# Kernel optimization log

Measured on AMD Instinct MI355X. Metric: run time of the kernel, lower is better.

The kernel has to match this reference:

```python
import jax, jax.numpy as jnp
import numpy as np

B, S, HID = 2, 2048, 3072
NH, NKV, HD = 24, 8, 128  # num_heads, kv heads, head_dim
G = NH // NKV             # GQA group size = 3
SCALING = HD ** -0.5
LAYER_SCALING = 1.0       # sqrt(layer_number=1)


def setup_inputs() -> dict:
    key = jax.random.key(0)
    ks = jax.random.split(key, 10)
    std = 0.02
    inp = {
        "hidden_states": jax.random.normal(ks[0], (B, S, HID), jnp.float32),
        # additive causal mask: 0 on/below diag, -1e9 above
        "attention_mask": jnp.where(
            jnp.tril(jnp.ones((S, S), bool)), 0.0, -1e9
        ).astype(jnp.float32)[None, None],
        # torch nn.Linear layout: W is [out, in]
        "Wq": jax.random.normal(ks[1], (HID, HID), jnp.float32) * std,
        "bq": jnp.zeros((HID,), jnp.float32),
        "Wk": jax.random.normal(ks[2], (NKV * HD, HID), jnp.float32) * std,
        "bk": jnp.zeros((NKV * HD,), jnp.float32),
        "Wv": jax.random.normal(ks[3], (NKV * HD, HID), jnp.float32) * std,
        "bv": jnp.zeros((NKV * HD,), jnp.float32),
        "Wd": jax.random.normal(ks[4], (HID, HID), jnp.float32) * std,
        "bd": jnp.zeros((HID,), jnp.float32),
    }
    return inp


def reference(hidden_states, attention_mask, Wq, bq, Wk, bk, Wv, bv, Wd, bd):
    b, s, _ = hidden_states.shape
    q = hidden_states @ Wq.T + bq                     # [B,S,HID]
    k = hidden_states @ Wk.T + bk                     # [B,S,NKV*HD]
    v = hidden_states @ Wv.T + bv
    # grouped layout: q [B,NKV,G,S,D]; repeat_interleave(dim=1) == grouped kv head
    q = q.reshape(b, s, NKV, G, HD).transpose(0, 2, 3, 1, 4)
    k = k.reshape(b, s, NKV, HD).transpose(0, 2, 1, 3)  # [B,NKV,S,D]
    v = v.reshape(b, s, NKV, HD).transpose(0, 2, 1, 3)
    scores = jnp.einsum("bhgqd,bhkd->bhgqk", q, k)
    scores = scores * (SCALING / LAYER_SCALING)
    scores = scores + attention_mask[:, :, None]       # broadcast over kv-head/group
    probs = jax.nn.softmax(scores.astype(jnp.float32), axis=-1).astype(scores.dtype)
    ctx = jnp.einsum("bhgqk,bhkd->bhgqd", probs, v)    # [B,NKV,G,S,D]
    # (kv_head, group) flattened == repeat_interleave head ordering
    ctx = ctx.transpose(0, 3, 1, 2, 4).reshape(b, s, HID)
    return ctx @ Wd.T + bd
```

## Files before the change

### kernel.cpp

```cpp
#include <hip/hip_runtime.h>

typedef unsigned short ushort_t;
typedef unsigned int uint32;
typedef __bf16 bf16x8 __attribute__((ext_vector_type(8)));
typedef float f32x4 __attribute__((ext_vector_type(4)));
typedef float f32x16 __attribute__((ext_vector_type(16)));

#define MFMA16(a, b, c) __builtin_amdgcn_mfma_f32_16x16x32_bf16((a), (b), (c), 0, 0, 0)
#define MFMA32(a, b, c) __builtin_amdgcn_mfma_f32_32x32x16_bf16((a), (b), (c), 0, 0, 0)

__device__ __forceinline__ ushort_t f2bf(float f) {
  union { float f; uint32 u; } c; c.f = f;
  uint32 u = c.u;
  u += 0x7fffu + ((u >> 16) & 1u);
  return (ushort_t)(u >> 16);
}

__device__ __forceinline__ void gload_lds16(const void* g, void* l) {
  __builtin_amdgcn_global_load_lds(
      (const __attribute__((address_space(1))) void*)g,
      (__attribute__((address_space(3))) void*)l, 16, 0, 0);
}

__global__ __launch_bounds__(256)
void cvt5_kernel(const float* __restrict__ p0, const float* __restrict__ p1,
                 const float* __restrict__ p2, const float* __restrict__ p3,
                 const float* __restrict__ p4, ushort_t* __restrict__ out) {
  const size_t B0 = 12582912;
  const size_t B1 = B0 + 9437184;
  const size_t B2 = B1 + 3145728;
  const size_t B3 = B2 + 3145728;
  const size_t B4 = B3 + 9437184;
  const size_t step = (size_t)gridDim.x * 256 * 4;
  for (size_t g = ((size_t)blockIdx.x * 256 + threadIdx.x) * 4; g < B4; g += step) {
    const float* src; size_t off;
    if (g < B0)      { src = p0; off = 0;  }
    else if (g < B1) { src = p1; off = B0; }
    else if (g < B2) { src = p2; off = B1; }
    else if (g < B3) { src = p3; off = B2; }
    else             { src = p4; off = B3; }
    float4 v = *(const float4*)(src + (g - off));
    union { uint2 u; ushort_t s[4]; } p;
    p.s[0] = f2bf(v.x); p.s[1] = f2bf(v.y);
    p.s[2] = f2bf(v.z); p.s[3] = f2bf(v.w);
    *(uint2*)(out + g) = p.u;
  }
}

#define GEMM_BODY32(ABASE, WROWBASE, KD)                                        \
  f32x16 acc[2][2] = {};                                                        \
  const int l31 = lane & 31;                                                    \
  const int khb = (lane >> 5) << 4;            \
  const int nk = (KD) >> 6;                                                     \
  for (int kt = 0; kt < nk; ++kt) {                                             \
    _Pragma("unroll")                                                           \
    for (int i = 0; i < 4; ++i) {                                               \
      int o = (i * 256 + tid) * 16;                                             \
      int row = o >> 7;                                                         \
      int src = (o & 127) ^ ((row & 7) << 4);                                   \
      gload_lds16(ABASE + (rowA0 + row) * (KD) + kt * 64 + (src >> 1),          \
                  (char*)As + o);                                               \
      gload_lds16(WROWBASE + (size_t)row * (KD) + kt * 64 + (src >> 1),         \
                  (char*)Bs + o);                                               \
    }                                                                           \
    __syncthreads();                                                            \
    _Pragma("unroll")                                                           \
    for (int ks = 0; ks < 4; ++ks) {                                            \
      bf16x8 af[2], bfr[2];                                                     \
      _Pragma("unroll")                                                         \
      for (int mi = 0; mi < 2; ++mi) {                                          \
        int ar = wr * 64 + mi * 32 + l31;                                       \
        int off = ar * 128 + ((ks * 32 + khb) ^ ((ar & 7) << 4));               \
        af[mi] = *(const bf16x8*)((const char*)As + off);                       \
      }                                                                         \
      _Pragma("unroll")                                                         \
      for (int nj = 0; nj < 2; ++nj) {                                          \
        int br = wc * 64 + nj * 32 + l31;                                       \
        int off = br * 128 + ((ks * 32 + khb) ^ ((br & 7) << 4));               \
        bfr[nj] = *(const bf16x8*)((const char*)Bs + off);                      \
      }                                                                         \
      _Pragma("unroll")                                                         \
      for (int mi = 0; mi < 2; ++mi)                                            \
        _Pragma("unroll")                                                       \
        for (int nj = 0; nj < 2; ++nj)                                          \
          acc[mi][nj] = MFMA32(af[mi], bfr[nj], acc[mi][nj]);                   \
    }                                                                           \
    __syncthreads();                                                            \
  }

__global__ __launch_bounds__(256)
void qkv_gemm_kernel(const ushort_t* __restrict__ A,
                     const ushort_t* __restrict__ Wq, const ushort_t* __restrict__ Wk,
                     const ushort_t* __restrict__ Wv,
                     const float* __restrict__ bq, const float* __restrict__ bk,
                     const float* __restrict__ bv, ushort_t* __restrict__ C)
{
  __shared__ __attribute__((aligned(16))) ushort_t As[128 * 64];
  __shared__ __attribute__((aligned(16))) ushort_t Bs[128 * 64];
  const int tid = threadIdx.x;
  const int lane = tid & 63;
  const int wv_ = tid >> 6;
  const int wr = wv_ >> 1, wc = wv_ & 1;
  const int x = blockIdx.x & 7;
  const int li = blockIdx.x >> 3;
  const int bm = ((x & 1) << 4) | (li & 15);
  const int bn = (x >> 1) * 10 + (li >> 4);

  const ushort_t* Wsrc; const float* bsrc; int nloc;
  if (bn < 24)      { Wsrc = Wq; bsrc = bq; nloc = bn << 7; }
  else if (bn < 32) { Wsrc = Wk; bsrc = bk; nloc = (bn - 24) << 7; }
  else              { Wsrc = Wv; bsrc = bv; nloc = (bn - 32) << 7; }

  const size_t rowA0 = (size_t)bm * 128;
  const ushort_t* Wrow = Wsrc + (size_t)nloc * 3072;

  GEMM_BODY32(A, Wrow, 3072)

  const int rhi = (lane >> 5) << 2;
#pragma unroll
  for (int nj = 0; nj < 2; ++nj) {
    int cl = wc * 64 + nj * 32 + l31;
    float bvl = bsrc[nloc + cl];
    int col = bn * 128 + cl;
#pragma unroll
    for (int mi = 0; mi < 2; ++mi) {
      int row0 = bm * 128 + wr * 64 + mi * 32 + rhi;
#pragma unroll
      for (int r = 0; r < 16; ++r) {
        int rowl = (r & 3) + 8 * (r >> 2);
        C[(size_t)(row0 + rowl) * 5120 + col] = f2bf(acc[mi][nj][r] + bvl);
      }
    }
  }
}

template <bool OUT_F32>
__global__ __launch_bounds__(256)
void gemm_bt_kernel(const ushort_t* __restrict__ A, const ushort_t* __restrict__ W,
                    const float* __restrict__ bias, void* __restrict__ Cv,
                    int N, int Kd, int cbn)
{
  __shared__ __attribute__((aligned(16))) ushort_t As[128 * 64];
  __shared__ __attribute__((aligned(16))) ushort_t Bs[128 * 64];
  const int tid = threadIdx.x;
  const int lane = tid & 63;
  const int wv_ = tid >> 6;
  const int wr = wv_ >> 1, wc = wv_ & 1;
  const int x = blockIdx.x & 7;
  const int li = blockIdx.x >> 3;
  const int bm = ((x & 1) << 4) | (li & 15);
  const int bn = (x >> 1) * cbn + (li >> 4);

  const size_t rowA0 = (size_t)bm * 128;
  const ushort_t* Wrow = W + (size_t)(bn * 128) * Kd;

  GEMM_BODY32(A, Wrow, Kd)

  const int rhi = (lane >> 5) << 2;
#pragma unroll
  for (int nj = 0; nj < 2; ++nj) {
    int col = bn * 128 + wc * 64 + nj * 32 + l31;
    float bvl = bias[col];
#pragma unroll
    for (int mi = 0; mi < 2; ++mi) {
      int row0 = bm * 128 + wr * 64 + mi * 32 + rhi;
#pragma unroll
      for (int r = 0; r < 16; ++r) {
        int rowl = (r & 3) + 8 * (r >> 2);
        float v = acc[mi][nj][r] + bvl;
        if (OUT_F32) ((float*)Cv)[(size_t)(row0 + rowl) * N + col] = v;
        else         ((ushort_t*)Cv)[(size_t)(row0 + rowl) * N + col] = f2bf(v);
      }
    }
  }
}

#define NHEADS 24
#define GRP 3
#define SEQ 2048
#define QSCL 0.12751745f
#define DTHR 8.0f

__global__ __launch_bounds__(256)
void attn_kernel(const ushort_t* __restrict__ QKV, ushort_t* __restrict__ O)
{
  __shared__ __attribute__((aligned(16))) ushort_t Kl[2][64 * 128];
  __shared__ __attribute__((aligned(16))) ushort_t Vt[128 * 64];

  const int tid = threadIdx.x;
  const int lane = tid & 63;
  const int wv = tid >> 6;
  const int l15 = lane & 15, lg = lane >> 4;
  const int bh = blockIdx.x;
  const int qb = 31 - blockIdx.y;
  const int b = bh / NHEADS, h = bh % NHEADS;
  const int kvh = h / GRP;
  const size_t kbase = (size_t)b * SEQ * 5120 + 3072 + (size_t)kvh * 128;
  const size_t vbase = kbase + 1024;
  const int q0 = qb * 64;

  const int kv4 = (tid & 15) * 4;
  const int d8 = (tid >> 4) * 8;
  const int a_sel = lg >> 1;
  const int s0l = (lane & 15) + 32 * (lg & 1);

#pragma unroll
  for (int i = 0; i < 4; ++i) {
    int o = (i * 256 + tid) * 16;
    int row = o >> 8;
    int src = (o & 255) ^ ((row & 7) << 4);
    gload_lds16(QKV + kbase + (size_t)row * 5120 + (src >> 1), (char*)&Kl[0][0] + o);
  }
  uint4 vr0, vr1, vr2, vr3;
  {
    const ushort_t* vg = QKV + vbase + (size_t)kv4 * 5120 + d8;
    vr0 = *(const uint4*)(vg);
    vr1 = *(const uint4*)(vg + 5120);
    vr2 = *(const uint4*)(vg + 10240);
    vr3 = *(const uint4*)(vg + 15360);
  }

  bf16x8 qf[4];
  {
    const ushort_t* qg = QKV + (size_t)(b * SEQ + q0 + wv * 16 + l15) * 5120 + h * 128 + lg * 8;
#pragma unroll
    for (int c = 0; c < 4; ++c) {
      bf16x8 q = *(const bf16x8*)(qg + c * 32);
#pragma unroll
      for (int e = 0; e < 8; ++e) q[e] = (__bf16)((float)q[e] * QSCL);
      qf[c] = q;
    }
  }

  float m_st = -1e30f, l_st = 0.f;
  f32x4 accO[8] = {};

  for (int t = 0; t <= qb; ++t) {
    const int cur = t & 1;
    {
      union { uint4 u; ushort_t s[8]; } L0, L1, L2, L3;
      L0.u = vr0; L1.u = vr1; L2.u = vr2; L3.u = vr3;
#pragma unroll
      for (int dd = 0; dd < 8; ++dd) {
        int d = d8 + dd;
        uint2 w;
        w.x = (uint32)L0.s[dd] | ((uint32)L1.s[dd] << 16);
        w.y = (uint32)L2.s[dd] | ((uint32)L3.s[dd] << 16);
        int swz = ((d & 7) ^ ((d >> 3) & 3)) << 4;
        int off = (d * 128 + kv4 * 2) ^ swz;
        *(uint2*)((char*)Vt + off) = w;
      }
    }
    asm volatile("s_waitcnt lgkmcnt(0)" ::: "memory");
    __builtin_amdgcn_s_barrier();

    if (t < qb) {
      const int kvn = (t + 1) * 64;
#pragma unroll
      for (int i = 0; i < 4; ++i) {
        int o = (i * 256 + tid) * 16;
        int row = o >> 8;
        int src = (o & 255) ^ ((row & 7) << 4);
        gload_lds16(QKV + kbase + (size_t)(kvn + row) * 5120 + (src >> 1),
                    (char*)&Kl[cur ^ 1][0] + o);
      }
      const ushort_t* vg = QKV + vbase + (size_t)(kvn + kv4) * 5120 + d8;
      vr0 = *(const uint4*)(vg);
      vr1 = *(const uint4*)(vg + 5120);
      vr2 = *(const uint4*)(vg + 10240);
      vr3 = *(const uint4*)(vg + 15360);
    }

    f32x4 s[4];
    __builtin_amdgcn_s_setprio(1);
#pragma unroll
    for (int n = 0; n < 4; ++n) {
      f32x4 z = {0.f, 0.f, 0.f, 0.f};
      s[n] = z;
#pragma unroll
      for (int c = 0; c < 4; ++c) {
        int row = n * 16 + l15;
        int boff = (row * 256 + c * 64 + lg * 16) ^ ((row & 7) << 4);
        bf16x8 kf = *(const bf16x8*)((const char*)Kl[cur] + boff);
        s[n] = MFMA16(kf, qf[c], s[n]);
      }
    }
    __builtin_amdgcn_s_setprio(0);

    if (t == qb) {
      const int qg_ = wv * 16 + l15;
#pragma unroll
      for (int n = 0; n < 4; ++n)
#pragma unroll
        for (int r = 0; r < 4; ++r)
          if (n * 16 + lg * 4 + r > qg_) s[n][r] = -1e9f;
    }

    float mx = fmaxf(fmaxf(fmaxf(s[0][0], s[0][1]), fmaxf(s[0][2], s[0][3])),
                     fmaxf(fmaxf(s[1][0], s[1][1]), fmaxf(s[1][2], s[1][3])));
    mx = fmaxf(mx, fmaxf(fmaxf(fmaxf(s[2][0], s[2][1]), fmaxf(s[2][2], s[2][3])),
                         fmaxf(fmaxf(s[3][0], s[3][1]), fmaxf(s[3][2], s[3][3]))));
    mx = fmaxf(mx, __shfl_xor(mx, 16, 64));
    mx = fmaxf(mx, __shfl_xor(mx, 32, 64));

    if (!__all(mx <= m_st + DTHR)) {
      const float mnew = fmaxf(m_st, mx);
      const float alpha = __builtin_amdgcn_exp2f(m_st - mnew);
      m_st = mnew;
      l_st *= alpha;
#pragma unroll
      for (int j = 0; j < 8; ++j)
#pragma unroll
        for (int r = 0; r < 4; ++r) accO[j][r] *= alpha;
    }

    float rsum = 0.f;
    uint32 dwA[4], dwB[4];
#pragma unroll
    for (int n = 0; n < 4; ++n) {
      float p0 = __builtin_amdgcn_exp2f(s[n][0] - m_st);
      float p1 = __builtin_amdgcn_exp2f(s[n][1] - m_st);
      float p2 = __builtin_amdgcn_exp2f(s[n][2] - m_st);
      float p3 = __builtin_amdgcn_exp2f(s[n][3] - m_st);
      rsum += (p0 + p1) + (p2 + p3);
      dwA[n] = (uint32)f2bf(p0) | ((uint32)f2bf(p1) << 16);
      dwB[n] = (uint32)f2bf(p2) | ((uint32)f2bf(p3) << 16);
    }
    rsum += __shfl_xor(rsum, 16, 64);
    rsum += __shfl_xor(rsum, 32, 64);
    l_st += rsum;

#pragma unroll
    for (int c = 0; c < 2; ++c) {
      uint32 xA0 = __shfl((int)dwA[2 * c],     s0l,      64);
      uint32 xB0 = __shfl((int)dwB[2 * c],     s0l,      64);
      uint32 xA1 = __shfl((int)dwA[2 * c + 1], s0l,      64);
      uint32 xB1 = __shfl((int)dwB[2 * c + 1], s0l,      64);
      uint32 yA0 = __shfl((int)dwA[2 * c],     s0l + 16, 64);
      uint32 yB0 = __shfl((int)dwB[2 * c],     s0l + 16, 64);
      uint32 yA1 = __shfl((int)dwA[2 * c + 1], s0l + 16, 64);
      uint32 yB1 = __shfl((int)dwB[2 * c + 1], s0l + 16, 64);
      union { uint4 u; bf16x8 v; } pb;
      pb.u.x = a_sel ? xA1 : xA0;
      pb.u.y = a_sel ? xB1 : xB0;
      pb.u.z = a_sel ? yA1 : yA0;
      pb.u.w = a_sel ? yB1 : yB0;
      __builtin_amdgcn_s_setprio(1);
#pragma unroll
      for (int j = 0; j < 8; ++j) {
        int d = j * 16 + l15;
        int swz = ((d & 7) ^ ((d >> 3) & 3)) << 4;
        int off = (d * 128 + c * 64 + lg * 16) ^ swz;
        bf16x8 vf = *(const bf16x8*)((const char*)Vt + off);
        accO[j] = MFMA16(vf, pb.v, accO[j]);
      }
      __builtin_amdgcn_s_setprio(0);
    }
    __builtin_amdgcn_s_barrier();
  }

  const float inv = 1.0f / l_st;
  ushort_t* og = O + (size_t)(b * SEQ + q0 + wv * 16 + l15) * 3072 + h * 128 + lg * 4;
#pragma unroll
  for (int j = 0; j < 8; ++j) {
    union { uint2 u; ushort_t s[4]; } w;
    w.s[0] = f2bf(accO[j][0] * inv);
    w.s[1] = f2bf(accO[j][1] * inv);
    w.s[2] = f2bf(accO[j][2] * inv);
    w.s[3] = f2bf(accO[j][3] * inv);
    *(uint2*)(og + j * 16) = w.u;
  }
}

extern "C" void kernel_launch(void* const* d_in, const int* in_sizes, int n_in,
                              void* d_out, int out_size, void* d_ws, size_t ws_size,
                              hipStream_t stream) {
  const float* hs = (const float*)d_in[0];
  const float* Wq = (const float*)d_in[2];
  const float* bq = (const float*)d_in[3];
  const float* Wk = (const float*)d_in[4];
  const float* bk = (const float*)d_in[5];
  const float* Wv = (const float*)d_in[6];
  const float* bv = (const float*)d_in[7];
  const float* Wd = (const float*)d_in[8];
  const float* bd = (const float*)d_in[9];
  float* out = (float*)d_out;

  const size_t N_HS = (size_t)4096 * 3072;
  const size_t N_WQ = (size_t)3072 * 3072;
  const size_t N_WK = (size_t)1024 * 3072;

  ushort_t* hs_bf = (ushort_t*)d_ws;
  ushort_t* Wq_bf = hs_bf + N_HS;
  ushort_t* Wk_bf = Wq_bf + N_WQ;
  ushort_t* Wv_bf = Wk_bf + N_WK;
  ushort_t* Wd_bf = Wv_bf + N_WK;
  ushort_t* QKVw  = Wd_bf + N_WQ;
  ushort_t* Cw    = hs_bf;

  cvt5_kernel<<<dim3(2048), dim3(256), 0, stream>>>(hs, Wq, Wk, Wv, Wd, hs_bf);
  qkv_gemm_kernel<<<dim3(1280), dim3(256), 0, stream>>>(hs_bf, Wq_bf, Wk_bf, Wv_bf,
                                                        bq, bk, bv, QKVw);
  attn_kernel<<<dim3(48, 32), dim3(256), 0, stream>>>(QKVw, Cw);
  gemm_bt_kernel<true><<<dim3(24 * 32), dim3(256), 0, stream>>>(Cw, Wd_bf, bd, out,
                                                                3072, 3072, 6);
}
```

Measured before the change: 395.2 us.

## Permute K rows in LDS so QK^T output feeds PV MFMA without shuffles

Loads K tile rows into LDS in a permuted order (kperm), so each lane's S accumulator elements already sit in the B-operand layout the P·V MFMA expects. This removes the eight cross-lane shuffles and selects per chunk, and the causal mask index is recomputed to match the permuted key order. It also swaps the manual f2bf rounding for native __bf16 conversions in the P packing and the output store. The risk is a wrong permutation or mask mapping, which would silently corrupt the attention result.

```diff
diff --git a/kernel.cpp b/kernel.cpp
--- a/kernel.cpp
+++ b/kernel.cpp
@@ -181,6 +181,10 @@
 #define QSCL 0.12751745f
 #define DTHR 8.0f
 
+__device__ __forceinline__ int kperm(int u) {
+  return 8 * ((u >> 2) & 3) + 4 * ((u >> 4) & 1) + (u & 3) + 32 * (u >> 5);
+}
+
 __global__ __launch_bounds__(256)
 void attn_kernel(const ushort_t* __restrict__ QKV, ushort_t* __restrict__ O)
 {
@@ -201,15 +205,14 @@
 
   const int kv4 = (tid & 15) * 4;
   const int d8 = (tid >> 4) * 8;
-  const int a_sel = lg >> 1;
-  const int s0l = (lane & 15) + 32 * (lg & 1);
 
 #pragma unroll
   for (int i = 0; i < 4; ++i) {
     int o = (i * 256 + tid) * 16;
     int row = o >> 8;
     int src = (o & 255) ^ ((row & 7) << 4);
-    gload_lds16(QKV + kbase + (size_t)row * 5120 + (src >> 1), (char*)&Kl[0][0] + o);
+    gload_lds16(QKV + kbase + (size_t)kperm(row) * 5120 + (src >> 1),
+                (char*)&Kl[0][0] + o);
   }
   uint4 vr0, vr1, vr2, vr3;
   {
@@ -261,7 +264,7 @@
         int o = (i * 256 + tid) * 16;
         int row = o >> 8;
         int src = (o & 255) ^ ((row & 7) << 4);
-        gload_lds16(QKV + kbase + (size_t)(kvn + row) * 5120 + (src >> 1),
+        gload_lds16(QKV + kbase + (size_t)(kvn + kperm(row)) * 5120 + (src >> 1),
                     (char*)&Kl[cur ^ 1][0] + o);
       }
       const ushort_t* vg = QKV + vbase + (size_t)(kvn + kv4) * 5120 + d8;
@@ -289,11 +292,14 @@
 
     if (t == qb) {
       const int qg_ = wv * 16 + l15;
+      const int blg = 8 * lg;
 #pragma unroll
       for (int n = 0; n < 4; ++n)
 #pragma unroll
-        for (int r = 0; r < 4; ++r)
-          if (n * 16 + lg * 4 + r > qg_) s[n][r] = -1e9f;
+        for (int r = 0; r < 4; ++r) {
+          int kvr = blg + ((n & 1) << 2) + r + ((n >> 1) << 5);
+          if (kvr > qg_) s[n][r] = -1e9f;
+        }
     }
 
     float mx = fmaxf(fmaxf(fmaxf(s[0][0], s[0][1]), fmaxf(s[0][2], s[0][3])),
@@ -315,16 +321,13 @@
     }
 
     float rsum = 0.f;
-    uint32 dwA[4], dwB[4];
 #pragma unroll
     for (int n = 0; n < 4; ++n) {
-      float p0 = __builtin_amdgcn_exp2f(s[n][0] - m_st);
-      float p1 = __builtin_amdgcn_exp2f(s[n][1] - m_st);
-      float p2 = __builtin_amdgcn_exp2f(s[n][2] - m_st);
-      float p3 = __builtin_amdgcn_exp2f(s[n][3] - m_st);
-      rsum += (p0 + p1) + (p2 + p3);
-      dwA[n] = (uint32)f2bf(p0) | ((uint32)f2bf(p1) << 16);
-      dwB[n] = (uint32)f2bf(p2) | ((uint32)f2bf(p3) << 16);
+      s[n][0] = __builtin_amdgcn_exp2f(s[n][0] - m_st);
+      s[n][1] = __builtin_amdgcn_exp2f(s[n][1] - m_st);
+      s[n][2] = __builtin_amdgcn_exp2f(s[n][2] - m_st);
+      s[n][3] = __builtin_amdgcn_exp2f(s[n][3] - m_st);
+      rsum += (s[n][0] + s[n][1]) + (s[n][2] + s[n][3]);
     }
     rsum += __shfl_xor(rsum, 16, 64);
     rsum += __shfl_xor(rsum, 32, 64);
@@ -332,19 +335,10 @@
 
 #pragma unroll
     for (int c = 0; c < 2; ++c) {
-      uint32 xA0 = __shfl((int)dwA[2 * c],     s0l,      64);
-      uint32 xB0 = __shfl((int)dwB[2 * c],     s0l,      64);
-      uint32 xA1 = __shfl((int)dwA[2 * c + 1], s0l,      64);
-      uint32 xB1 = __shfl((int)dwB[2 * c + 1], s0l,      64);
-      uint32 yA0 = __shfl((int)dwA[2 * c],     s0l + 16, 64);
-      uint32 yB0 = __shfl((int)dwB[2 * c],     s0l + 16, 64);
-      uint32 yA1 = __shfl((int)dwA[2 * c + 1], s0l + 16, 64);
-      uint32 yB1 = __shfl((int)dwB[2 * c + 1], s0l + 16, 64);
-      union { uint4 u; bf16x8 v; } pb;
-      pb.u.x = a_sel ? xA1 : xA0;
-      pb.u.y = a_sel ? xB1 : xB0;
-      pb.u.z = a_sel ? yA1 : yA0;
-      pb.u.w = a_sel ? yB1 : yB0;
+      bf16x8 pb;
+#pragma unroll
+      for (int j = 0; j < 8; ++j)
+        pb[j] = (__bf16)s[(c << 1) | (j >> 2)][j & 3];
       __builtin_amdgcn_s_setprio(1);
 #pragma unroll
       for (int j = 0; j < 8; ++j) {
@@ -352,7 +346,7 @@
         int swz = ((d & 7) ^ ((d >> 3) & 3)) << 4;
         int off = (d * 128 + c * 64 + lg * 16) ^ swz;
         bf16x8 vf = *(const bf16x8*)((const char*)Vt + off);
-        accO[j] = MFMA16(vf, pb.v, accO[j]);
+        accO[j] = MFMA16(vf, pb, accO[j]);
       }
       __builtin_amdgcn_s_setprio(0);
     }
@@ -363,11 +357,11 @@
   ushort_t* og = O + (size_t)(b * SEQ + q0 + wv * 16 + l15) * 3072 + h * 128 + lg * 4;
 #pragma unroll
   for (int j = 0; j < 8; ++j) {
-    union { uint2 u; ushort_t s[4]; } w;
-    w.s[0] = f2bf(accO[j][0] * inv);
-    w.s[1] = f2bf(accO[j][1] * inv);
-    w.s[2] = f2bf(accO[j][2] * inv);
-    w.s[3] = f2bf(accO[j][3] * inv);
+    union { __bf16 h[4]; uint2 u; } w;
+    w.h[0] = (__bf16)(accO[j][0] * inv);
+    w.h[1] = (__bf16)(accO[j][1] * inv);
+    w.h[2] = (__bf16)(accO[j][2] * inv);
+    w.h[3] = (__bf16)(accO[j][3] * inv);
     *(uint2*)(og + j * 16) = w.u;
   }
 }
```

After: 379.3 us (median of 3 runs). 1.04x faster.
